# Kernel optimization log

Measured on AMD Instinct MI355X. Metric: run time of the kernel, lower is better.

Reference implementation:

```python
import jax, jax.numpy as jnp
import numpy as np

EPS = 1e-5
NEG = jnp.float32(-1e30)


def _mha(q_in, kv, in_w, in_b, out_w, out_b, n_heads, allowed=None):
    # torch nn.MultiheadAttention (batch_first, eval mode)
    B, Nq, D = q_in.shape
    hd = D // n_heads
    wq, wk, wv = jnp.split(in_w, 3, axis=0)
    bq, bk, bv = jnp.split(in_b, 3)
    q = (q_in @ wq.T + bq).reshape(B, Nq, n_heads, hd).transpose(0, 2, 1, 3)
    k = (kv @ wk.T + bk).reshape(B, -1, n_heads, hd).transpose(0, 2, 1, 3)
    v = (kv @ wv.T + bv).reshape(B, -1, n_heads, hd).transpose(0, 2, 1, 3)
    s = jnp.einsum('bhqd,bhkd->bhqk', q, k) / jnp.sqrt(jnp.float32(hd))
    if allowed is not None:
        s = jnp.where(allowed[:, None, :, :], s, NEG)
    a = jax.nn.softmax(s, axis=-1)
    o = jnp.einsum('bhqk,bhkd->bhqd', a, v).transpose(0, 2, 1, 3).reshape(B, Nq, D)
    o = o @ out_w.T + out_b
    if allowed is not None:
        # rows with no allowed keys: torch would NaN; we zero them (deterministic)
        o = jnp.where(allowed.any(-1)[..., None], o, 0.0)
    return o


def _layernorm(x, g, b):
    mu = x.mean(-1, keepdims=True)
    var = ((x - mu) ** 2).mean(-1, keepdims=True)
    return (x - mu) * jax.lax.rsqrt(var + EPS) * g + b


def setup_inputs() -> dict:
    key = jax.random.key(0)
    B, N, D, NH = 128, 128, 512, 8
    ks = jax.random.split(key, 16)
    s = 0.02
    return {
        'H': jax.random.normal(ks[0], (B, N, D), jnp.float32),
        'pred_heads': jax.random.randint(ks[1], (B, N), 0, N, jnp.int32),
        'mask': jnp.ones((B, N), jnp.int32),
        'head_in_w': jax.random.normal(ks[2], (3 * D, D)) * s,
        'head_in_b': jnp.zeros((3 * D,), jnp.float32),
        'head_out_w': jax.random.normal(ks[3], (D, D)) * s,
        'head_out_b': jnp.zeros((D,), jnp.float32),
        'sib_in_w': jax.random.normal(ks[4], (3 * D, D)) * s,
        'sib_in_b': jnp.zeros((3 * D,), jnp.float32),
        'sib_out_w': jax.random.normal(ks[5], (D, D)) * s,
        'sib_out_b': jnp.zeros((D,), jnp.float32),
        'child_w': jax.random.normal(ks[6], (D, 2 * D)) * s,
        'child_b': jnp.zeros((D,), jnp.float32),
        'gate_w': jax.random.normal(ks[7], (D, 4 * D)) * s,
        'gate_b': jnp.zeros((D,), jnp.float32),
        'trans_w': jax.random.normal(ks[8], (D, 4 * D)) * s,
        'trans_b': jnp.zeros((D,), jnp.float32),
        'ln_g': jnp.ones((D,), jnp.float32),
        'ln_b': jnp.zeros((D,), jnp.float32),
    }


def reference(H, pred_heads, mask, head_in_w, head_in_b, head_out_w, head_out_b,
              sib_in_w, sib_in_b, sib_out_w, sib_out_b, child_w, child_b,
              gate_w, gate_b, trans_w, trans_b, ln_g, ln_b):
    B, N, D = H.shape
    NH = 8
    heads = jnp.clip(pred_heads, 0, N - 1)  # [B,N]
    maskb = mask.astype(bool)

    # 1) head message: gather each node's head repr, attend Q=H, K=V=head_repr
    head_repr = jnp.take_along_axis(H, heads[..., None], axis=1)  # [B,N,D]
    head_msg = _mha(H, head_repr, head_in_w, head_in_b, head_out_w, head_out_b, NH)

    # 2) child aggregation: vectorized scatter-add replacing the Python loop.
    # loop runs d in [1, length) with mask a prefix -> valid = mask & (d >= 1)
    valid = maskb & (jnp.arange(N) >= 1)  # [B,N]
    contrib = H * valid[..., None].astype(H.dtype)
    flat_idx = (jnp.arange(B)[:, None] * N + heads).reshape(-1)
    child_sum = jnp.zeros((B * N, D), H.dtype).at[flat_idx].add(
        contrib.reshape(B * N, D)).reshape(B, N, D)
    child_count = jnp.zeros((B * N,), H.dtype).at[flat_idx].add(
        valid.reshape(-1).astype(H.dtype)).reshape(B, N, 1)
    child_avg = child_sum / jnp.maximum(child_count, 1.0)
    child_msg = jax.nn.gelu(
        jnp.concatenate([H, child_avg], -1) @ child_w.T + child_b,
        approximate=False)

    # 3) sibling attention (N <= 128 branch): same head, not self, both masked-in
    same_head = heads[:, :, None] == heads[:, None, :]
    eye = jnp.eye(N, dtype=bool)[None]
    allowed = same_head & ~eye & maskb[:, None, :] & maskb[:, :, None]
    sib_msg = _mha(H, H, sib_in_w, sib_in_b, sib_out_w, sib_out_b, NH, allowed=allowed)

    # 4) gated fusion + residual + layernorm
    combined = jnp.concatenate([H, head_msg, child_msg, sib_msg], -1)
    gate = jax.nn.sigmoid(combined @ gate_w.T + gate_b)
    update = jax.nn.gelu(combined @ trans_w.T + trans_b, approximate=False)
    return _layernorm(H + gate * update, ln_g, ln_b)
```

## Files before the change

### kernel.cpp

```cpp
#include <hip/hip_runtime.h>
#include <hip/hip_bf16.h>

typedef __bf16 bf16x8 __attribute__((ext_vector_type(8)));
typedef float f32x4 __attribute__((ext_vector_type(4)));

__device__ __forceinline__ void gload16(const void* g, void* l) {
  __builtin_amdgcn_global_load_lds(
      (const __attribute__((address_space(1))) unsigned int*)g,
      (__attribute__((address_space(3))) unsigned int*)l, 16, 0, 0);
}

__device__ __forceinline__ float gelu_f(float x) {
  return 0.5f * x * (1.f + erff(x * 0.70710678118654752f));
}
__device__ __forceinline__ float sigmoid_f(float x) {
  return 1.f / (1.f + __expf(-x));
}

template<int EPI, bool OBF16>
__global__ __launch_bounds__(256)
void gemm_kernel(const __hip_bfloat16* __restrict__ A0, int lda0,
                 const __hip_bfloat16* __restrict__ A1, int lda1,
                 const __hip_bfloat16* __restrict__ A2, int lda2,
                 int ks1, int ks2,
                 const __hip_bfloat16* __restrict__ B, int ldb,
                 const float* __restrict__ bias,
                 const float* __restrict__ fvec,
                 const float* __restrict__ flags,
                 void* __restrict__ C, int ldc, int K)
{
  __shared__ __align__(16) __hip_bfloat16 As[128 * 32];
  __shared__ __align__(16) __hip_bfloat16 Bs[128 * 32];
  const int t = threadIdx.x;
  const int l = t & 63, w = t >> 6;
  const int gx = gridDim.x;
  int bid = blockIdx.y * gx + blockIdx.x;
  {
    const int nwg = gx * gridDim.y;
    const int xcd = bid & 7, rk = bid >> 3, q = nwg >> 3, r = nwg & 7;
    bid = (xcd < r ? xcd * (q + 1) : r * (q + 1) + (xcd - r) * q) + rk;
  }
  const int m0 = (bid / gx) * 128, n0 = (bid % gx) * 128;
  const int wm = (w >> 1) * 64, wn = (w & 1) * 64;
  const int l15 = l & 15, lg = l >> 4;

  const int r0 = t >> 2;
  const int kk0 = ((t & 3) ^ ((t >> 3) & 3)) * 8;
  char* lA = (char*)As + t * 16;
  char* lB = (char*)Bs + t * 16;
  const size_t boff1 = (size_t)(n0 + r0) * ldb + kk0;
  const size_t boff2 = (size_t)(n0 + r0 + 64) * ldb + kk0;

  int aoffR[4], boffR[4];
#pragma unroll
  for (int i = 0; i < 4; ++i) {
    const int ra = wm + i * 16 + l15;
    aoffR[i] = ra * 32 + ((lg ^ ((ra >> 1) & 3)) * 8);
    const int rb = wn + i * 16 + l15;
    boffR[i] = rb * 32 + ((lg ^ ((rb >> 1) & 3)) * 8);
  }
  f32x4 acc[4][4] = {};

#pragma unroll 1
  for (int seg = 0; seg < 3; ++seg) {
    const __hip_bfloat16* Ap;
    int ldA, kb, ke;
    if (seg == 0)      { Ap = A0; ldA = lda0; kb = 0;   ke = ks1; }
    else if (seg == 1) { Ap = A1; ldA = lda1; kb = ks1; ke = ks2; }
    else               { Ap = A2; ldA = lda2; kb = ks2; ke = K;   }
    if (kb >= ke) continue;
    const size_t aoff1 = (size_t)(m0 + r0) * ldA + kk0;
    const size_t aoff2 = (size_t)(m0 + r0 + 64) * ldA + kk0;
    for (int k0 = kb; k0 < ke; k0 += 32) {
      const int kr = k0 - kb;
      gload16(Ap + aoff1 + kr, lA);
      gload16(Ap + aoff2 + kr, lA + 4096);
      gload16(B + boff1 + k0, lB);
      gload16(B + boff2 + k0, lB + 4096);
      __syncthreads();
      bf16x8 af[4], bfr[4];
#pragma unroll
      for (int i = 0; i < 4; ++i) {
        af[i]  = *(const bf16x8*)((const __hip_bfloat16*)As + aoffR[i]);
        bfr[i] = *(const bf16x8*)((const __hip_bfloat16*)Bs + boffR[i]);
      }
#pragma unroll
      for (int mi = 0; mi < 4; ++mi)
#pragma unroll
        for (int ni = 0; ni < 4; ++ni)
          acc[mi][ni] = __builtin_amdgcn_mfma_f32_16x16x32_bf16(af[mi], bfr[ni], acc[mi][ni], 0, 0, 0);
      __syncthreads();
    }
  }

  if (EPI == 2) {
#pragma unroll
    for (int mi = 0; mi < 4; ++mi) {
#pragma unroll
      for (int nh = 0; nh < 2; ++nh) {
        const int ni = nh * 2;
        const int sc = n0 + wn + ni * 16;
        const float bg = bias[sc + l15], bt = bias[sc + 16 + l15];
        const float fg = fvec[sc + l15], ft = fvec[sc + 16 + l15];
        const int ocol = (sc >> 5) * 16 + l15;
#pragma unroll
        for (int j = 0; j < 4; ++j) {
          const int row = m0 + wm + mi * 16 + lg * 4 + j;
          const float flg = flags[row];
          float g  = acc[mi][ni][j]     + bg + flg * fg;
          float tv = acc[mi][ni + 1][j] + bt + flg * ft;
          ((float*)C)[(size_t)row * ldc + ocol] = sigmoid_f(g) * gelu_f(tv);
        }
      }
    }
    return;
  }
#pragma unroll
  for (int mi = 0; mi < 4; ++mi)
#pragma unroll
    for (int ni = 0; ni < 4; ++ni) {
      const int col = n0 + wn + ni * 16 + l15;
      const float bc = bias ? bias[col] : 0.f;
#pragma unroll
      for (int j = 0; j < 4; ++j) {
        const int row = m0 + wm + mi * 16 + lg * 4 + j;
        float v = acc[mi][ni][j] + bc;
        if (EPI == 1) v = gelu_f(v);
        if (OBF16) ((__hip_bfloat16*)C)[(size_t)row * ldc + col] = __float2bfloat16(v);
        else       ((float*)C)[(size_t)row * ldc + col] = v;
      }
    }
}

template<bool SIB>
__global__ __launch_bounds__(256)
void attn_kernel(const __hip_bfloat16* __restrict__ QKV,
                 const int* __restrict__ pred_heads,
                 const int* __restrict__ mask,
                 __hip_bfloat16* __restrict__ Oout, int ldo,
                 float* __restrict__ flags,
                 int qofs)
{
  __shared__ __align__(16) __hip_bfloat16 smem[128 * 128];
  __shared__ __align__(16) __hip_bfloat16 Vt[64 * 128];
  __shared__ int hs[128];
  __shared__ int mk[128];
  const int b = blockIdx.x >> 3, h = blockIdx.x & 7;
  const int t = threadIdx.x, l = t & 63, w = t >> 6;
  const int l15 = l & 15, lg = l >> 4;
  __hip_bfloat16* Qs = smem;
  __hip_bfloat16* Ks = smem + 128 * 64;

  if (t < 128) {
    int hh = pred_heads[b * 128 + t];
    hh = hh < 0 ? 0 : (hh > 127 ? 127 : hh);
    hs[t] = hh;
    mk[t] = mask[b * 128 + t];
  }
  __syncthreads();
  const size_t tb = (size_t)b * 128 * 3072;
  const int co = qofs + h * 64;
#pragma unroll
  for (int it = 0; it < 4; ++it) {
    const int idx = it * 256 + t;
    const int row = idx >> 3;
    const int c8 = (idx & 7) * 8;
    const int sl = ((c8 >> 3) ^ (row & 7)) * 8;
    *(uint4*)(Qs + row * 64 + sl) = *(const uint4*)(QKV + tb + (size_t)row * 3072 + co + c8);
    const int krow = SIB ? row : hs[row];
    *(uint4*)(Ks + row * 64 + sl) = *(const uint4*)(QKV + tb + (size_t)krow * 3072 + co + 512 + c8);
    uint4 vv = *(const uint4*)(QKV + tb + (size_t)krow * 3072 + co + 1024 + c8);
    const __hip_bfloat16* vp = (const __hip_bfloat16*)&vv;
#pragma unroll
    for (int u = 0; u < 8; ++u) {
      const int d = c8 + u;
      Vt[d * 128 + (((row >> 3) ^ (d & 7)) * 8) + (row & 7)] = vp[u];
    }
  }
  __syncthreads();

  const int r0 = w * 32;
  f32x4 s[2][8] = {};
  const int x7 = l15 & 7;
#pragma unroll
  for (int ks = 0; ks < 2; ++ks) {
    const int sl = ((ks * 4 + lg) ^ x7) * 8;
    bf16x8 qa0 = *(const bf16x8*)(Qs + (r0 + l15) * 64 + sl);
    bf16x8 qa1 = *(const bf16x8*)(Qs + (r0 + 16 + l15) * 64 + sl);
#pragma unroll
    for (int nj = 0; nj < 8; ++nj) {
      bf16x8 kb = *(const bf16x8*)(Ks + (nj * 16 + l15) * 64 + sl);
      s[0][nj] = __builtin_amdgcn_mfma_f32_16x16x32_bf16(qa0, kb, s[0][nj], 0, 0, 0);
      s[1][nj] = __builtin_amdgcn_mfma_f32_16x16x32_bf16(qa1, kb, s[1][nj], 0, 0, 0);
    }
  }
  const float scale = 0.125f;
  float inv_sum[2][4];
#pragma unroll
  for (int mi = 0; mi < 2; ++mi) {
#pragma unroll
    for (int j = 0; j < 4; ++j) {
      const int row = r0 + mi * 16 + lg * 4 + j;
      float mx = -1e30f;
#pragma unroll
      for (int nj = 0; nj < 8; ++nj) {
        float v = s[mi][nj][j] * scale;
        bool ok = true;
        if (SIB) {
          int c = nj * 16 + l15;
          ok = (hs[row] == hs[c]) && (row != c) && mk[row] && mk[c];
        }
        mx = fmaxf(mx, ok ? v : -1e30f);
      }
#pragma unroll
      for (int m = 1; m < 16; m <<= 1) mx = fmaxf(mx, __shfl_xor(mx, m));
      float sum = 0.f;
#pragma unroll
      for (int nj = 0; nj < 8; ++nj) {
        float v = s[mi][nj][j] * scale;
        bool ok = true;
        if (SIB) {
          int c = nj * 16 + l15;
          ok = (hs[row] == hs[c]) && (row != c) && mk[row] && mk[c];
        }
        float p = ok ? __expf(v - mx) : 0.f;
        s[mi][nj][j] = p;
        sum += p;
      }
#pragma unroll
      for (int m = 1; m < 16; m <<= 1) sum += __shfl_xor(sum, m);
      inv_sum[mi][j] = sum > 0.f ? 1.f / sum : 0.f;
    }
  }
  __syncthreads();
#pragma unroll
  for (int mi = 0; mi < 2; ++mi)
#pragma unroll
    for (int nj = 0; nj < 8; ++nj)
#pragma unroll
      for (int j = 0; j < 4; ++j) {
        const int rr = r0 + mi * 16 + lg * 4 + j;
        const int cc = nj * 16 + l15;
        smem[rr * 128 + (((cc >> 3) ^ (rr & 7)) * 8) + (cc & 7)] = __float2bfloat16(s[mi][nj][j]);
      }
  __syncthreads();

  f32x4 o[2][4] = {};
#pragma unroll
  for (int js = 0; js < 4; ++js) {
    const int slot = js * 4 + lg;
    const int slp = (slot ^ x7) * 8;
    bf16x8 pa0 = *(const bf16x8*)(smem + (r0 + l15) * 128 + slp);
    bf16x8 pa1 = *(const bf16x8*)(smem + (r0 + 16 + l15) * 128 + slp);
#pragma unroll
    for (int dj = 0; dj < 4; ++dj) {
      bf16x8 vb = *(const bf16x8*)(Vt + (dj * 16 + l15) * 128 + slp);
      o[0][dj] = __builtin_amdgcn_mfma_f32_16x16x32_bf16(pa0, vb, o[0][dj], 0, 0, 0);
      o[1][dj] = __builtin_amdgcn_mfma_f32_16x16x32_bf16(pa1, vb, o[1][dj], 0, 0, 0);
    }
  }
  const int hb = h * 64;
#pragma unroll
  for (int mi = 0; mi < 2; ++mi)
#pragma unroll
    for (int dj = 0; dj < 4; ++dj)
#pragma unroll
      for (int j = 0; j < 4; ++j) {
        const int row = r0 + mi * 16 + lg * 4 + j;
        const int dc = dj * 16 + l15;
        const float val = o[mi][dj][j] * inv_sum[mi][j];
        Oout[(size_t)(b * 128 + row) * ldo + hb + dc] = __float2bfloat16(val);
      }
  if (SIB && h == 0 && l15 == 0) {
#pragma unroll
    for (int mi = 0; mi < 2; ++mi)
#pragma unroll
      for (int j = 0; j < 4; ++j) {
        const int row = r0 + mi * 16 + lg * 4 + j;
        flags[b * 128 + row] = inv_sum[mi][j] > 0.f ? 1.f : 0.f;
      }
  }
}

__global__ __launch_bounds__(256)
void child_kernel(const float* __restrict__ H,
                  const int* __restrict__ pred_heads,
                  const int* __restrict__ mask,
                  __hip_bfloat16* __restrict__ Cavg)
{
  __shared__ float sum[128 * 64];
  __shared__ int cnt[128];
  __shared__ int hsl[128];
  __shared__ int vld[128];
  const int t = threadIdx.x;
  const int b = blockIdx.y, ch = blockIdx.x;
#pragma unroll
  for (int u = 0; u < 32; ++u) sum[u * 256 + t] = 0.f;
  if (t < 128) {
    int hh = pred_heads[b * 128 + t];
    hh = hh < 0 ? 0 : (hh > 127 ? 127 : hh);
    hsl[t] = hh;
    vld[t] = (mask[b * 128 + t] != 0) && (t >= 1);
    cnt[t] = 0;
  }
  __syncthreads();
  if (t < 128 && vld[t]) atomicAdd(&cnt[hsl[t]], 1);
  __syncthreads();
  const int c = t & 63;
  const int isub = t >> 6;
  for (int ii = 0; ii < 32; ++ii) {
    int i = ii * 4 + isub;
    if (vld[i]) atomicAdd(&sum[hsl[i] * 64 + c], H[((size_t)b * 128 + i) * 512 + ch * 64 + c]);
  }
  __syncthreads();
#pragma unroll
  for (int u = 0; u < 32; ++u) {
    int idx = u * 256 + t;
    int p = idx >> 6, cc = idx & 63;
    float avg = sum[idx] / fmaxf((float)cnt[p], 1.f);
    Cavg[((size_t)b * 128 + p) * 512 + ch * 64 + cc] = __float2bfloat16(avg);
  }
}

__global__ void conv_all_kernel(const float* __restrict__ s0, const float* __restrict__ s1,
                                const float* __restrict__ s2, const float* __restrict__ s3,
                                __hip_bfloat16* __restrict__ d0, __hip_bfloat16* __restrict__ d1,
                                __hip_bfloat16* __restrict__ d2, __hip_bfloat16* __restrict__ d3)
{
  int gid = blockIdx.x * 256 + threadIdx.x;
  const float* s; __hip_bfloat16* d; int i;
  if      (gid <  196608) { s = s0; d = d0; i = gid; }
  else if (gid <  393216) { s = s1; d = d1; i = gid - 196608; }
  else if (gid <  524288) { s = s2; d = d2; i = gid - 393216; }
  else                    { s = s3; d = d3; i = gid - 524288; }
  i *= 4;
  float4 v = *(const float4*)(s + i);
  union { __hip_bfloat16 h[4]; uint2 u; } p;
  p.h[0] = __float2bfloat16(v.x); p.h[1] = __float2bfloat16(v.y);
  p.h[2] = __float2bfloat16(v.z); p.h[3] = __float2bfloat16(v.w);
  *(uint2*)(d + i) = p.u;
}

__global__ void convT_kernel(const float* __restrict__ a, const float* __restrict__ b,
                             __hip_bfloat16* __restrict__ ta, __hip_bfloat16* __restrict__ tb)
{
  int idx = blockIdx.x * 256 + threadIdx.x;
  const float* s = a; __hip_bfloat16* d = ta;
  if (idx >= 262144) { s = b; d = tb; idx -= 262144; }
  int i = idx >> 9, j = idx & 511;
  d[i * 512 + j] = __float2bfloat16(s[(size_t)j * 512 + i]);
}

__global__ void build_gt_kernel(const float* __restrict__ gw, const float* __restrict__ tw,
                                const float* __restrict__ gb, const float* __restrict__ tb,
                                __hip_bfloat16* __restrict__ Wf, __hip_bfloat16* __restrict__ Whin,
                                __hip_bfloat16* __restrict__ Wsin, float* __restrict__ bias)
{
  int idx = blockIdx.x * 256 + threadIdx.x;
  int s = idx >> 11, c = idx & 2047;
  int q = s >> 5, r = s & 31;
  float v = (r < 16) ? gw[(size_t)(q * 16 + r) * 2048 + c]
                     : tw[(size_t)(q * 16 + r - 16) * 2048 + c];
  __hip_bfloat16 hv = __float2bfloat16(v);
  if      (c <  512) Wf[(size_t)s * 2048 + c] = hv;
  else if (c < 1024) Whin[(size_t)s * 512 + (c - 512)] = hv;
  else if (c < 1536) Wf[(size_t)s * 2048 + (c - 512)] = hv;
  else               Wsin[(size_t)s * 512 + (c - 1536)] = hv;
  if (c == 0) bias[s] = (r < 16) ? gb[q * 16 + r] : tb[q * 16 + r - 16];
}

__global__ __launch_bounds__(256)
void foldbias_kernel(const __hip_bfloat16* __restrict__ Whin, const __hip_bfloat16* __restrict__ Wsin,
                     const float* __restrict__ hob, const float* __restrict__ sob,
                     float* __restrict__ bias_gt, float* __restrict__ fvec)
{
  const int s = blockIdx.x * 256 + threadIdx.x;
  float a = 0.f, c = 0.f;
  for (int j = 0; j < 512; j += 8) {
    bf16x8 wh = *(const bf16x8*)(Whin + (size_t)s * 512 + j);
    bf16x8 wsv = *(const bf16x8*)(Wsin + (size_t)s * 512 + j);
#pragma unroll
    for (int u = 0; u < 8; ++u) {
      a += (float)wh[u] * hob[j + u];
      c += (float)wsv[u] * sob[j + u];
    }
  }
  bias_gt[s] += a;
  fvec[s] = c;
}

__global__ __launch_bounds__(64)
void ln_kernel(const float* __restrict__ H, const float* __restrict__ U,
               const float* __restrict__ g, const float* __restrict__ bta,
               float* __restrict__ out)
{
  const int row = blockIdx.x, l = threadIdx.x;
  const size_t hb = (size_t)row * 512;
  float x[8];
  float sum = 0.f;
#pragma unroll
  for (int u = 0; u < 8; ++u) {
    int d = u * 64 + l;
    float val = H[hb + d] + U[hb + d];
    x[u] = val; sum += val;
  }
#pragma unroll
  for (int m = 32; m; m >>= 1) sum += __shfl_xor(sum, m);
  float mean = sum * (1.f / 512.f);
  float vs = 0.f;
#pragma unroll
  for (int u = 0; u < 8; ++u) { float d0 = x[u] - mean; vs += d0 * d0; }
#pragma unroll
  for (int m = 32; m; m >>= 1) vs += __shfl_xor(vs, m);
  float rstd = rsqrtf(vs * (1.f / 512.f) + 1e-5f);
#pragma unroll
  for (int u = 0; u < 8; ++u) {
    int d = u * 64 + l;
    out[hb + d] = (x[u] - mean) * rstd * g[d] + bta[d];
  }
}

extern "C" void kernel_launch(void* const* d_in, const int* in_sizes, int n_in,
                              void* d_out, int out_size, void* d_ws, size_t ws_size,
                              hipStream_t stream)
{
  (void)in_sizes; (void)n_in; (void)out_size; (void)ws_size;
  const float* H      = (const float*)d_in[0];
  const int*  pred    = (const int*)d_in[1];
  const int*  maskp   = (const int*)d_in[2];
  const float* hin_w  = (const float*)d_in[3];
  const float* hin_b  = (const float*)d_in[4];
  const float* hout_w = (const float*)d_in[5];
  const float* hout_b = (const float*)d_in[6];
  const float* sin_w  = (const float*)d_in[7];
  const float* sin_b  = (const float*)d_in[8];
  const float* sout_w = (const float*)d_in[9];
  const float* sout_b = (const float*)d_in[10];
  const float* ch_w   = (const float*)d_in[11];
  const float* ch_b   = (const float*)d_in[12];
  const float* g_w    = (const float*)d_in[13];
  const float* g_b    = (const float*)d_in[14];
  const float* t_w    = (const float*)d_in[15];
  const float* t_b    = (const float*)d_in[16];
  const float* lng    = (const float*)d_in[17];
  const float* lnb    = (const float*)d_in[18];

  char* ws = (char*)d_ws;
  __hip_bfloat16* Wqkv  = (__hip_bfloat16*)(ws + 0);
  __hip_bfloat16* Wch   = (__hip_bfloat16*)(ws + 3145728);
  __hip_bfloat16* Wgt   = (__hip_bfloat16*)(ws + 4194304);
  float* bias_qkv       = (float*)(ws + 8388608);
  float* bias_gt        = (float*)(ws + 8400896);
  float* fvec           = (float*)(ws + 8404992);
  float* flags          = (float*)(ws + 8409088);
  __hip_bfloat16* Hbf   = (__hip_bfloat16*)(ws + 8474624);
  char* QKVr            = ws + 25251840;
  __hip_bfloat16* QKV   = (__hip_bfloat16*)QKVr;
  __hip_bfloat16* Whin  = (__hip_bfloat16*)(QKVr + 0);
  __hip_bfloat16* Wsin  = (__hip_bfloat16*)(QKVr + 1048576);
  __hip_bfloat16* WhoT  = (__hip_bfloat16*)(QKVr + 2097152);
  __hip_bfloat16* WsoT  = (__hip_bfloat16*)(QKVr + 2621440);
  __hip_bfloat16* CHM   = (__hip_bfloat16*)(QKVr + 0);
  float* U              = (float*)(QKVr + 16777216);
  __hip_bfloat16* Cavg  = (__hip_bfloat16*)(QKVr + 50331648);
  __hip_bfloat16* CM2   = (__hip_bfloat16*)(ws + 125915136);

  conv_all_kernel<<<10240, 256, 0, stream>>>(hin_w, sin_w, ch_w, H,
                                             Wqkv, Wqkv + 786432, Wch, Hbf);
  build_gt_kernel<<<8192, 256, 0, stream>>>(g_w, t_w, g_b, t_b, Wgt, Whin, Wsin, bias_gt);
  convT_kernel<<<2048, 256, 0, stream>>>(hout_w, sout_w, WhoT, WsoT);
  foldbias_kernel<<<4, 256, 0, stream>>>(Whin, Wsin, hout_b, sout_b, bias_gt, fvec);
  hipMemcpyAsync(bias_qkv, hin_b, 1536 * 4, hipMemcpyDeviceToDevice, stream);
  hipMemcpyAsync(bias_qkv + 1536, sin_b, 1536 * 4, hipMemcpyDeviceToDevice, stream);

  gemm_kernel<0, true><<<dim3(4, 8), 256, 0, stream>>>(
      Whin, 512, Whin, 512, Whin, 512, 512, 512, WhoT, 512,
      (const float*)nullptr, (const float*)nullptr, (const float*)nullptr,
      (void*)(Wgt + 1024), 2048, 512);
  gemm_kernel<0, true><<<dim3(4, 8), 256, 0, stream>>>(
      Wsin, 512, Wsin, 512, Wsin, 512, 512, 512, WsoT, 512,
      (const float*)nullptr, (const float*)nullptr, (const float*)nullptr,
      (void*)(Wgt + 1536), 2048, 512);

  gemm_kernel<0, true><<<dim3(24, 128), 256, 0, stream>>>(
      Hbf, 512, Hbf, 512, Hbf, 512, 512, 512, Wqkv, 512,
      bias_qkv, (const float*)nullptr, (const float*)nullptr,
      (void*)QKV, 3072, 512);

  attn_kernel<false><<<1024, 256, 0, stream>>>(QKV, pred, maskp, CM2, 1024, flags, 0);
  attn_kernel<true><<<1024, 256, 0, stream>>>(QKV, pred, maskp, CM2 + 512, 1024, flags, 1536);

  child_kernel<<<dim3(8, 128), 256, 0, stream>>>(H, pred, maskp, Cavg);
  gemm_kernel<1, true><<<dim3(4, 128), 256, 0, stream>>>(
      Hbf, 512, Cavg, 512, Cavg, 512, 512, 1024, Wch, 1024,
      ch_b, (const float*)nullptr, (const float*)nullptr,
      (void*)CHM, 512, 1024);

  gemm_kernel<2, false><<<dim3(8, 128), 256, 0, stream>>>(
      Hbf, 512, CHM, 512, CM2, 1024, 512, 1024, Wgt, 2048,
      bias_gt, fvec, flags, (void*)U, 512, 2048);

  ln_kernel<<<16384, 64, 0, stream>>>(H, U, lng, lnb, (float*)d_out);
}
```

Baseline: 509.2 us.

## Add 256x256 multi-buffered GEMM kernel with XCD remap for QKV and gate GEMMs

Introduces a new 512-thread GEMM kernel with 256x256 output tiles, a 4-deep LDS ring of global-to-LDS prefetches, swizzled LDS layout, interleaved MFMA with prefetch issue and setprio, and an XCD-aware block remapping. It replaces the older 128x128 kernel for the large QKV projection and the gated fusion GEMM, aiming to raise data reuse and hide load latency. It needs 128KB dynamic LDS and many more accumulator registers, which limits occupancy and can hurt performance if the pipeline does not hide latency well.

```diff
diff --git a/kernel.cpp b/kernel.cpp
--- a/kernel.cpp
+++ b/kernel.cpp
@@ -15,6 +15,156 @@
 }
 __device__ __forceinline__ float sigmoid_f(float x) {
   return 1.f / (1.f + __expf(-x));
+}
+
+template<int EPI>
+__global__ __launch_bounds__(512, 2)
+void gemm8_kernel(const __hip_bfloat16* __restrict__ A0, int lda0,
+                  const __hip_bfloat16* __restrict__ A1, int lda1,
+                  const __hip_bfloat16* __restrict__ A2, int lda2,
+                  int ks1, int ks2,
+                  const __hip_bfloat16* __restrict__ B, int ldb,
+                  const float* __restrict__ bias,
+                  const float* __restrict__ fvec,
+                  const float* __restrict__ flags,
+                  void* __restrict__ C, int ldc, int K)
+{
+  extern __shared__ __align__(16) char lds[];
+  const int t = threadIdx.x;
+  const int l = t & 63;
+  const int w = t >> 6;
+  const int l15 = l & 15, lg = (l >> 4) & 3;
+  const int orig = blockIdx.y * gridDim.x + blockIdx.x;
+  const int nwg = gridDim.x * gridDim.y;
+  const int gy = gridDim.y;
+  const int xcd = orig & 7, rk = orig >> 3, q = nwg >> 3, r = nwg & 7;
+  const int bid = (xcd < r ? xcd * (q + 1) : r * (q + 1) + (xcd - r) * q) + rk;
+  const int m0 = (bid % gy) * 256;
+  const int n0 = (bid / gy) * 256;
+
+  const int srow = t >> 2;
+  const int kc8 = ((t & 3) ^ ((t >> 3) & 3)) * 8;
+  const int mbase = (w >> 2) * 128;
+  const int nbase = (w & 3) * 64;
+  const int swz = (l15 >> 1) & 3;
+  const int kslot = (lg ^ swz) * 8;
+  int aoff[8], boff[4];
+#pragma unroll
+  for (int mf = 0; mf < 8; ++mf) aoff[mf] = (mbase + mf * 16 + l15) * 32 + kslot;
+#pragma unroll
+  for (int nf = 0; nf < 4; ++nf) boff[nf] = (nbase + nf * 16 + l15) * 32 + kslot;
+
+  auto segA = [&](int k0, const __hip_bfloat16*& Ap, int& ldA, int& krel) {
+    if (k0 >= ks2)      { Ap = A2; ldA = lda2; krel = k0 - ks2; }
+    else if (k0 >= ks1) { Ap = A1; ldA = lda1; krel = k0 - ks1; }
+    else                { Ap = A0; ldA = lda0; krel = k0; }
+  };
+  auto stageA = [&](int buf, const __hip_bfloat16* Ap, int ldA, int krel) {
+    char* base = lds + buf * 32768 + t * 16;
+    gload16(Ap + (size_t)(m0 + srow) * ldA + krel + kc8, base);
+    gload16(Ap + (size_t)(m0 + 128 + srow) * ldA + krel + kc8, base + 8192);
+  };
+  auto stageB = [&](int buf, int k0) {
+    char* base = lds + buf * 32768 + 16384 + t * 16;
+    gload16(B + (size_t)(n0 + srow) * ldb + k0 + kc8, base);
+    gload16(B + (size_t)(n0 + 128 + srow) * ldb + k0 + kc8, base + 8192);
+  };
+
+  f32x4 acc[8][4] = {};
+  const int NT = K >> 5;
+
+#pragma unroll 1
+  for (int pt = 0; pt < 3; ++pt) {
+    const __hip_bfloat16* Ap; int ldA, krel;
+    segA(pt * 32, Ap, ldA, krel);
+    stageA(pt, Ap, ldA, krel);
+    stageB(pt, pt * 32);
+  }
+  asm volatile("s_waitcnt vmcnt(8)" ::: "memory");
+  __builtin_amdgcn_s_barrier();
+  __builtin_amdgcn_sched_barrier(0);
+
+#pragma unroll 1
+  for (int tt = 0; tt < NT; ++tt) {
+    const int buf = tt & 3;
+    const __hip_bfloat16* As = (const __hip_bfloat16*)(lds + buf * 32768);
+    const __hip_bfloat16* Bs = (const __hip_bfloat16*)(lds + buf * 32768 + 16384);
+    const int pf = tt + 3;
+    const bool do_pf = pf < NT;
+    const int pbuf = pf & 3;
+    const __hip_bfloat16* Ap = A0; int ldA = lda0, krel = 0;
+    if (do_pf) segA(pf * 32, Ap, ldA, krel);
+
+    bf16x8 bv[4], av[4];
+#pragma unroll
+    for (int nf = 0; nf < 4; ++nf) bv[nf] = *(const bf16x8*)(Bs + boff[nf]);
+#pragma unroll
+    for (int mf = 0; mf < 4; ++mf) av[mf] = *(const bf16x8*)(As + aoff[mf]);
+    if (do_pf) stageA(pbuf, Ap, ldA, krel);
+    __builtin_amdgcn_s_setprio(1);
+#pragma unroll
+    for (int mf = 0; mf < 4; ++mf)
+#pragma unroll
+      for (int nf = 0; nf < 4; ++nf)
+        acc[mf][nf] = __builtin_amdgcn_mfma_f32_16x16x32_bf16(av[mf], bv[nf], acc[mf][nf], 0, 0, 0);
+    __builtin_amdgcn_s_setprio(0);
+
+#pragma unroll
+    for (int mf = 0; mf < 4; ++mf) av[mf] = *(const bf16x8*)(As + aoff[mf + 4]);
+    if (do_pf) stageB(pbuf, pf * 32);
+    __builtin_amdgcn_s_setprio(1);
+#pragma unroll
+    for (int mf = 0; mf < 4; ++mf)
+#pragma unroll
+      for (int nf = 0; nf < 4; ++nf)
+        acc[mf + 4][nf] = __builtin_amdgcn_mfma_f32_16x16x32_bf16(av[mf], bv[nf], acc[mf + 4][nf], 0, 0, 0);
+    __builtin_amdgcn_s_setprio(0);
+
+    __builtin_amdgcn_sched_barrier(0);
+    if (tt + 3 < NT)      asm volatile("s_waitcnt vmcnt(8)" ::: "memory");
+    else if (tt + 2 < NT) asm volatile("s_waitcnt vmcnt(4)" ::: "memory");
+    else if (tt + 1 < NT) asm volatile("s_waitcnt vmcnt(0)" ::: "memory");
+    if (tt + 1 < NT) {
+      __builtin_amdgcn_s_barrier();
+      __builtin_amdgcn_sched_barrier(0);
+    }
+  }
+
+  if (EPI == 2) {
+#pragma unroll
+    for (int mf = 0; mf < 8; ++mf) {
+#pragma unroll
+      for (int nh = 0; nh < 2; ++nh) {
+        const int nf = nh * 2;
+        const int sc = n0 + nbase + nf * 16;
+        const float bg = bias[sc + l15], bt = bias[sc + 16 + l15];
+        const float fg = fvec[sc + l15], ft = fvec[sc + 16 + l15];
+        const int ocol = (sc >> 5) * 16 + l15;
+#pragma unroll
+        for (int j = 0; j < 4; ++j) {
+          const int row = m0 + mbase + mf * 16 + lg * 4 + j;
+          const float flg = flags[row];
+          float g  = acc[mf][nf][j]     + bg + flg * fg;
+          float tv = acc[mf][nf + 1][j] + bt + flg * ft;
+          ((float*)C)[(size_t)row * ldc + ocol] = sigmoid_f(g) * gelu_f(tv);
+        }
+      }
+    }
+    return;
+  }
+#pragma unroll
+  for (int mf = 0; mf < 8; ++mf)
+#pragma unroll
+    for (int nf = 0; nf < 4; ++nf) {
+      const int col = n0 + nbase + nf * 16 + l15;
+      const float bc = bias ? bias[col] : 0.f;
+#pragma unroll
+      for (int j = 0; j < 4; ++j) {
+        const int row = m0 + mbase + mf * 16 + lg * 4 + j;
+        ((__hip_bfloat16*)C)[(size_t)row * ldc + col] =
+            __float2bfloat16(acc[mf][nf][j] + bc);
+      }
+    }
 }
 
 template<int EPI, bool OBF16>
@@ -93,28 +243,6 @@
     }
   }
 
-  if (EPI == 2) {
-#pragma unroll
-    for (int mi = 0; mi < 4; ++mi) {
-#pragma unroll
-      for (int nh = 0; nh < 2; ++nh) {
-        const int ni = nh * 2;
-        const int sc = n0 + wn + ni * 16;
-        const float bg = bias[sc + l15], bt = bias[sc + 16 + l15];
-        const float fg = fvec[sc + l15], ft = fvec[sc + 16 + l15];
-        const int ocol = (sc >> 5) * 16 + l15;
-#pragma unroll
-        for (int j = 0; j < 4; ++j) {
-          const int row = m0 + wm + mi * 16 + lg * 4 + j;
-          const float flg = flags[row];
-          float g  = acc[mi][ni][j]     + bg + flg * fg;
-          float tv = acc[mi][ni + 1][j] + bt + flg * ft;
-          ((float*)C)[(size_t)row * ldc + ocol] = sigmoid_f(g) * gelu_f(tv);
-        }
-      }
-    }
-    return;
-  }
 #pragma unroll
   for (int mi = 0; mi < 4; ++mi)
 #pragma unroll
@@ -465,6 +593,11 @@
   __hip_bfloat16* Cavg  = (__hip_bfloat16*)(QKVr + 50331648);
   __hip_bfloat16* CM2   = (__hip_bfloat16*)(ws + 125915136);
 
+  hipFuncSetAttribute(reinterpret_cast<const void*>(gemm8_kernel<0>),
+                      hipFuncAttributeMaxDynamicSharedMemorySize, 131072);
+  hipFuncSetAttribute(reinterpret_cast<const void*>(gemm8_kernel<2>),
+                      hipFuncAttributeMaxDynamicSharedMemorySize, 131072);
+
   conv_all_kernel<<<10240, 256, 0, stream>>>(hin_w, sin_w, ch_w, H,
                                              Wqkv, Wqkv + 786432, Wch, Hbf);
   build_gt_kernel<<<8192, 256, 0, stream>>>(g_w, t_w, g_b, t_b, Wgt, Whin, Wsin, bias_gt);
@@ -482,7 +615,7 @@
       (const float*)nullptr, (const float*)nullptr, (const float*)nullptr,
       (void*)(Wgt + 1536), 2048, 512);
 
-  gemm_kernel<0, true><<<dim3(24, 128), 256, 0, stream>>>(
+  gemm8_kernel<0><<<dim3(12, 64), 512, 131072, stream>>>(
       Hbf, 512, Hbf, 512, Hbf, 512, 512, 512, Wqkv, 512,
       bias_qkv, (const float*)nullptr, (const float*)nullptr,
       (void*)QKV, 3072, 512);
@@ -496,7 +629,7 @@
       ch_b, (const float*)nullptr, (const float*)nullptr,
       (void*)CHM, 512, 1024);
 
-  gemm_kernel<2, false><<<dim3(8, 128), 256, 0, stream>>>(
+  gemm8_kernel<2><<<dim3(4, 64), 512, 131072, stream>>>(
       Hbf, 512, CHM, 512, CM2, 1024, 512, 1024, Wgt, 2048,
       bias_gt, fvec, flags, (void*)U, 512, 2048);
 
```

New measurement: 488.5 us. 1.04x faster.
